# Kernel optimization log

Hardware: AMD Instinct MI355X
Metric: run time of the kernel (lower is better)

Reference implementation:

```python
import jax, jax.numpy as jnp
import numpy as np

B, S, CL, DIM, HEADS, FFN = 2, 2048, 512, 2048, 16, 8192
EPS = 1e-6


def rms_norm(x, w):
    return x * jax.lax.rsqrt(jnp.mean(x * x, axis=-1, keepdims=True) + EPS) * w


def mha(q, k, v, num_heads):
    b, sq, d = q.shape
    sk = k.shape[1]
    hd = d // num_heads
    q = q.reshape(b, sq, num_heads, hd)
    k = k.reshape(b, sk, num_heads, hd)
    v = v.reshape(b, sk, num_heads, hd)
    attn = jnp.einsum('bqhd,bkhd->bhqk', q, k) * (hd ** -0.5)
    attn = jax.nn.softmax(attn, axis=-1)
    out = jnp.einsum('bhqk,bkhd->bqhd', attn, v)
    return out.reshape(b, sq, d)


def setup_inputs() -> dict:
    key = jax.random.key(0)
    ks = iter(jax.random.split(key, 48))
    nrm = lambda shape, scale: jax.random.normal(next(ks), shape, jnp.float32) * scale
    w_scale = DIM ** -0.5
    inp = {
        'x': nrm((B, S, DIM), 1.0),
        'e': nrm((B, 6, DIM), 0.5),
        'context': nrm((B, CL, DIM), 1.0),
        'modulation': nrm((1, 6, DIM), w_scale),
        'norm1_w': jnp.ones((DIM,), jnp.float32),
        'norm2_w': jnp.ones((DIM,), jnp.float32),
        'norm3_w': jnp.ones((DIM,), jnp.float32),
        'sa_nq_w': jnp.ones((DIM,), jnp.float32),
        'sa_nk_w': jnp.ones((DIM,), jnp.float32),
        'ffn_norm_w': jnp.ones((DIM,), jnp.float32),
        'sa_qw': nrm((DIM, DIM), w_scale), 'sa_qb': jnp.zeros((DIM,), jnp.float32),
        'sa_kw': nrm((DIM, DIM), w_scale), 'sa_kb': jnp.zeros((DIM,), jnp.float32),
        'sa_vw': nrm((DIM, DIM), w_scale), 'sa_vb': jnp.zeros((DIM,), jnp.float32),
        'sa_ow': nrm((DIM, DIM), w_scale), 'sa_ob': jnp.zeros((DIM,), jnp.float32),
        'ca_qw': nrm((DIM, DIM), w_scale), 'ca_qb': jnp.zeros((DIM,), jnp.float32),
        'ca_kw': nrm((DIM, DIM), w_scale), 'ca_kb': jnp.zeros((DIM,), jnp.float32),
        'ca_vw': nrm((DIM, DIM), w_scale), 'ca_vb': jnp.zeros((DIM,), jnp.float32),
        'ca_ow': nrm((DIM, DIM), w_scale), 'ca_ob': jnp.zeros((DIM,), jnp.float32),
        'ffn_w1': nrm((DIM, FFN), w_scale), 'ffn_b1': jnp.zeros((FFN,), jnp.float32),
        'ffn_w2': nrm((FFN, DIM), FFN ** -0.5), 'ffn_b2': jnp.zeros((DIM,), jnp.float32),
    }
    return inp


def reference(x, e, context, modulation, norm1_w, norm2_w, norm3_w, sa_nq_w, sa_nk_w,
              ffn_norm_w, sa_qw, sa_qb, sa_kw, sa_kb, sa_vw, sa_vb, sa_ow, sa_ob,
              ca_qw, ca_qb, ca_kw, ca_kb, ca_vw, ca_vb, ca_ow, ca_ob,
              ffn_w1, ffn_b1, ffn_w2, ffn_b2):
    # AdaLN modulation: (modulation + e) chunked into 6 along dim=1 -> each [B,1,DIM]
    mod = modulation + e
    e0, e1, e2, e3, e4, e5 = [mod[:, i:i + 1, :] for i in range(6)]

    # --- self attention with qk_norm=True ---
    h = rms_norm(x, norm1_w) * (1.0 + e1) + e0
    q = rms_norm(h @ sa_qw + sa_qb, sa_nq_w)
    k = rms_norm(h @ sa_kw + sa_kb, sa_nk_w)
    v = h @ sa_vw + sa_vb
    y = mha(q, k, v, HEADS) @ sa_ow + sa_ob
    x = x + y * e2

    # --- cross attention (cross_attn_norm=False, no qk norm) ---
    h = rms_norm(x, norm2_w)
    q = h @ ca_qw + ca_qb
    k = context @ ca_kw + ca_kb
    v = context @ ca_vw + ca_vb
    y = mha(q, k, v, HEADS) @ ca_ow + ca_ob
    x = x + y

    # --- FFN: modulate(norm3(x)) -> RMSNorm -> Linear -> GELU(tanh) -> Linear ---
    h = rms_norm(x, norm3_w) * (1.0 + e4) + e3
    h = rms_norm(h, ffn_norm_w)
    h = jax.nn.gelu(h @ ffn_w1 + ffn_b1, approximate=True)
    y = h @ ffn_w2 + ffn_b2
    x = x + y * e5
    return x
```

## Files before the change

### kernel.cpp

```cpp
#include <hip/hip_runtime.h>
#include <hip/hip_bf16.h>
#include <cstdint>

#define DIM   2048
#define HEADS 16
#define HD    128
#define SEQ   2048
#define CLEN  512
#define FFND  8192
#define BATCH 2

using bf16 = __hip_bfloat16;
typedef __attribute__((ext_vector_type(8))) short  short8;
typedef __attribute__((ext_vector_type(4))) short  short4v;
typedef __attribute__((ext_vector_type(4))) float  f32x4;
typedef __attribute__((ext_vector_type(8))) __bf16 bf16x8;

__device__ __forceinline__ short f2bs(float f){ bf16 h = __float2bfloat16(f); return __builtin_bit_cast(short, h); }
__device__ __forceinline__ float bs2f(short s){ return __builtin_bit_cast(float, (uint32_t)((uint16_t)s) << 16); }

__device__ __forceinline__ f32x4 mfma16(short8 a, short8 b, f32x4 c){
  return __builtin_amdgcn_mfma_f32_16x16x32_bf16(
      __builtin_bit_cast(bf16x8, a), __builtin_bit_cast(bf16x8, b), c, 0, 0, 0);
}

__device__ __forceinline__ void gload_lds16(const void* g, const void* l){
  __builtin_amdgcn_global_load_lds(
      (const __attribute__((address_space(1))) void*)(uintptr_t)g,
      (__attribute__((address_space(3))) void*)(uint32_t)(uintptr_t)l, 16, 0, 0);
}

__device__ __forceinline__ float block_sum(float v, float* sbuf, int tid){
  #pragma unroll
  for (int m = 32; m >= 1; m >>= 1) v += __shfl_xor(v, m, 64);
  const int w = tid >> 6;
  if ((tid & 63) == 0) sbuf[w] = v;
  __syncthreads();
  float r = sbuf[0] + sbuf[1] + sbuf[2] + sbuf[3];
  __syncthreads();
  return r;
}


__global__ void modadd_k(const float* __restrict__ m, const float* __restrict__ e,
                         float* __restrict__ out){
  int i = blockIdx.x * 256 + threadIdx.x;
  out[i] = m[i % (6 * DIM)] + e[i];
}

__global__ void f2b8_k(const float* __restrict__ in, bf16* __restrict__ out){
  int i = blockIdx.x * 256 + threadIdx.x;
  const float4* p = (const float4*)in;
  float4 a = p[2*i], c = p[2*i+1];
  short8 o;
  o[0]=f2bs(a.x); o[1]=f2bs(a.y); o[2]=f2bs(a.z); o[3]=f2bs(a.w);
  o[4]=f2bs(c.x); o[5]=f2bs(c.y); o[6]=f2bs(c.z); o[7]=f2bs(c.w);
  *((short8*)out + i) = o;
}

__global__ void biascat_k(const float* __restrict__ b0, const float* __restrict__ b1,
                          const float* __restrict__ b2, float* __restrict__ bcat){
  int i = blockIdx.x * 256 + threadIdx.x;
  const float* src = (i < DIM) ? b0 : (i < 2*DIM) ? b1 : b2;
  bcat[i] = src[i & (DIM-1)];
}

__global__ __launch_bounds__(256) void transpose_w(const float* __restrict__ W,
                                                   bf16* __restrict__ Wt, int K, int N){
  __shared__ float tile[32][33];
  const int tx = threadIdx.x & 31, ty = threadIdx.x >> 5;
  const size_t k0 = blockIdx.y * 32, n0 = blockIdx.x * 32;
  #pragma unroll
  for (int i = 0; i < 4; i++)
    tile[ty + i*8][tx] = W[(k0 + ty + i*8) * (size_t)N + n0 + tx];
  __syncthreads();
  #pragma unroll
  for (int i = 0; i < 4; i++)
    Wt[(n0 + ty + i*8) * (size_t)K + k0 + tx] = __float2bfloat16(tile[tx][ty + i*8]);
}

template<int MODE>
__global__ __launch_bounds__(256) void norm_x(const float* __restrict__ x,
    const float* __restrict__ w1, const float* __restrict__ w2,
    const float* __restrict__ mod, bf16* __restrict__ out, int S)
{
  const int row = blockIdx.x, tid = threadIdx.x;
  const int b = row / S;
  __shared__ float sbuf[4];
  const float* xr = x + (size_t)row * DIM;
  float v[8];
  #pragma unroll
  for (int i = 0; i < 2; i++){
    float4 t = *(const float4*)(xr + i*1024 + tid*4);
    v[i*4+0]=t.x; v[i*4+1]=t.y; v[i*4+2]=t.z; v[i*4+3]=t.w;
  }
  float ss = 0.f;
  #pragma unroll
  for (int j = 0; j < 8; j++) ss += v[j]*v[j];
  ss = block_sum(ss, sbuf, tid);
  const float r = rsqrtf(ss * (1.0f/DIM) + 1e-6f);
  const float* mb = mod + (size_t)b * 6 * DIM;
  float t8[8];
  #pragma unroll
  for (int i = 0; i < 2; i++)
    #pragma unroll
    for (int j = 0; j < 4; j++){
      int n = i*1024 + tid*4 + j;
      float val = v[i*4+j] * r * w1[n];
      if (MODE == 1) val = val * (1.f + mb[DIM + n]) + mb[n];
      if (MODE == 3) val = val * (1.f + mb[4*DIM + n]) + mb[3*DIM + n];
      t8[i*4+j] = val;
    }
  if (MODE == 3){
    float s2 = 0.f;
    #pragma unroll
    for (int j = 0; j < 8; j++) s2 += t8[j]*t8[j];
    s2 = block_sum(s2, sbuf, tid);
    const float r2 = rsqrtf(s2 * (1.0f/DIM) + 1e-6f);
    #pragma unroll
    for (int i = 0; i < 2; i++)
      #pragma unroll
      for (int j = 0; j < 4; j++){
        int n = i*1024 + tid*4 + j;
        t8[i*4+j] = t8[i*4+j] * r2 * w2[n];
      }
  }
  #pragma unroll
  for (int i = 0; i < 2; i++){
    short4v o;
    #pragma unroll
    for (int j = 0; j < 4; j++) o[j] = f2bs(t8[i*4+j]);
    *(short4v*)(out + (size_t)row*DIM + i*1024 + tid*4) = o;
  }
}

__global__ __launch_bounds__(256) void rmsnorm_bf16_ip(bf16* __restrict__ x,
                                                       const float* __restrict__ w){
  const int row = blockIdx.x, tid = threadIdx.x;
  __shared__ float sbuf[4];
  bf16* xr = x + (size_t)row * DIM;
  short8 v = *(const short8*)(xr + tid*8);
  float f[8]; float ss = 0.f;
  #pragma unroll
  for (int j = 0; j < 8; j++){ f[j] = bs2f(v[j]); ss += f[j]*f[j]; }
  ss = block_sum(ss, sbuf, tid);
  const float r = rsqrtf(ss * (1.0f/DIM) + 1e-6f);
  short8 o;
  #pragma unroll
  for (int j = 0; j < 8; j++) o[j] = f2bs(f[j] * r * w[tid*8 + j]);
  *(short8*)(xr + tid*8) = o;
}

#define GBUF 24576
template<int EPI>
__global__ __launch_bounds__(512, 2) void gemm_bf16(
    const bf16* __restrict__ A, const bf16* __restrict__ Bt,
    const float* __restrict__ bias, const float* __restrict__ xin,
    const float* __restrict__ mod, float* __restrict__ outf,
    bf16* __restrict__ outb, bf16* __restrict__ out1, bf16* __restrict__ out2,
    int M, int N, int K, int S_tok, int eidx)
{
  __shared__ __align__(16) char lds[3][GBUF];
  const int tid = threadIdx.x;
  const int w = tid >> 6, l = tid & 63;
  const int lrow = l & 15, lhi = l >> 4;
  const int wm = w >> 2, wn = w & 3;
  const size_t m0 = (size_t)blockIdx.y * 128, n0 = (size_t)blockIdx.x * 256;

  f32x4 acc[4][4] = {};

  auto gofs = [&](int sid){ return (size_t)(sid >> 2) * K + (size_t)(((sid & 3) ^ ((sid >> 3) & 3)) * 8); };
  const bf16* gA0 = A  + m0 * K + gofs(tid);
  const bf16* gB0 = Bt + n0 * K + gofs(tid);
  const bf16* gB1 = Bt + n0 * K + gofs(tid + 512);

  auto stage = [&](int kt, char* buf){
    const size_t ko = (size_t)kt * 32;
    gload_lds16(gA0 + ko, buf + tid * 16);
    gload_lds16(gB0 + ko, buf + 8192 + tid * 16);
    gload_lds16(gB1 + ko, buf + 8192 + (tid + 512) * 16);
  };

  const int nt = K >> 5;
  stage(0, lds[0]);
  stage(1, lds[1]);
  asm volatile("s_waitcnt vmcnt(3)" ::: "memory");
  __builtin_amdgcn_s_barrier();
  __builtin_amdgcn_sched_barrier(0);

  const int sread = (lhi ^ ((lrow >> 1) & 3)) * 16;

  int bi = 0;
  for (int t = 0; t < nt; ++t){
    const char* br = lds[bi];
    const bool st = (t + 2 < nt);
    if (st){
      int wi = bi + 2; if (wi >= 3) wi -= 3;
      stage(t + 2, lds[wi]);
    }
    short8 af[4], bf[4];
    #pragma unroll
    for (int mi = 0; mi < 4; mi++)
      af[mi] = *(const short8*)(br + (wm*64 + mi*16 + lrow)*64 + sread);
    #pragma unroll
    for (int ni = 0; ni < 4; ni++)
      bf[ni] = *(const short8*)(br + 8192 + (wn*64 + ni*16 + lrow)*64 + sread);
    __builtin_amdgcn_s_setprio(1);
    #pragma unroll
    for (int mi = 0; mi < 4; mi++)
      #pragma unroll
      for (int ni = 0; ni < 4; ni++)
        acc[mi][ni] = mfma16(af[mi], bf[ni], acc[mi][ni]);
    __builtin_amdgcn_s_setprio(0);
    if (st)               { asm volatile("s_waitcnt vmcnt(3)" ::: "memory"); }
    else if (t + 1 < nt)  { asm volatile("s_waitcnt vmcnt(0)" ::: "memory"); }
    __builtin_amdgcn_s_barrier();
    __builtin_amdgcn_sched_barrier(0);
    bi = (bi + 1 == 3) ? 0 : bi + 1;
  }

  #pragma unroll
  for (int mi = 0; mi < 4; mi++)
    #pragma unroll
    for (int ni = 0; ni < 4; ni++)
      #pragma unroll
      for (int r = 0; r < 4; r++){
        const size_t m = m0 + wm*64 + mi*16 + lhi*4 + r;
        const size_t n = n0 + wn*64 + ni*16 + lrow;
        float v = acc[mi][ni][r] + bias[n];
        if constexpr (EPI == 0) {
          outb[m * N + n] = __float2bfloat16(v);
        } else if constexpr (EPI == 1) {
          const size_t b = m / S_tok, s = m % S_tok;
          const size_t h = n >> 7, d = n & 127;
          outb[((b*HEADS + h)*HD + d) * S_tok + s] = __float2bfloat16(v);
        } else if constexpr (EPI == 2) {
          const float ev = mod[(m / S_tok) * 6 * DIM + (size_t)eidx * DIM + n];
          outf[m * N + n] = xin[m * N + n] + v * ev;
        } else if constexpr (EPI == 3) {
          outf[m * N + n] += v;
        } else if constexpr (EPI == 4) {
          float u = 0.7978845608028654f * (v + 0.044715f * v * v * v);
          outb[m * N + n] = __float2bfloat16(0.5f * v * (1.0f + tanhf(u)));
        } else {
          const size_t sg = n >> 11, col = n & 2047;
          if (sg == 0)      outb[m * DIM + col] = __float2bfloat16(v);
          else if (sg == 1) out1[m * DIM + col] = __float2bfloat16(v);
          else {
            const size_t b = m / S_tok, s = m % S_tok;
            const size_t h = col >> 7, d = col & 127;
            out2[((b*HEADS + h)*HD + d) * S_tok + s] = __float2bfloat16(v);
          }
        }
      }
}

__global__ __launch_bounds__(256, 2) void attn_fwd(
    const bf16* __restrict__ Q, const bf16* __restrict__ Kp, const bf16* __restrict__ Vt,
    bf16* __restrict__ O, int SQ, int SKV)
{
  const int tid = threadIdx.x, w = tid >> 6, l = tid & 63;
  const int lrow = l & 15, lhi = l >> 4;
  const int nwg = gridDim.x;
  const int p = blockIdx.x;
  const int f = (p & 7) * (nwg >> 3) + (p >> 3);
  const int nqb = SQ >> 6;
  const int xq = f % nqb;
  const int h  = (f / nqb) % HEADS;
  const int b  = f / (nqb * HEADS);
  const int q0 = xq * 64 + w * 16;

  __shared__ __align__(16) char kls[2][16384];
  __shared__ __align__(16) char vls[2][16384];
  __shared__ __align__(16) bf16 P[4][16][72];
  const float scale = 0.08838834764831845f;

  const bf16* qp = Q + ((size_t)(b*SQ + q0 + lrow))*DIM + h*HD + lhi*8;
  short8 qf[4];
  #pragma unroll
  for (int ds = 0; ds < 4; ds++) qf[ds] = *(const short8*)(qp + ds*32);

  const bf16* kg = Kp + (size_t)b*SKV*DIM + h*HD;
  const bf16* vg = Vt + (size_t)(b*HEADS + h)*HD*SKV;

  f32x4 acc[8] = {};
  float m_run = -INFINITY, l_run = 0.f;
  const int nt = SKV >> 6;

  auto stage = [&](int buf, int kv0){
    char* kd = &kls[buf][0];
    #pragma unroll
    for (int i = 0; i < 4; i++){
      int sid = i*256 + tid;
      int row = sid >> 4, sg = sid & 15;
      int gsg = sg ^ (row & 7);
      gload_lds16(kg + (size_t)(kv0 + row)*DIM + gsg*8, kd + sid*16);
    }
    char* vd = &vls[buf][0];
    #pragma unroll
    for (int i = 0; i < 4; i++){
      int sid = i*256 + tid;
      int d = sid >> 3, sg = sid & 7;
      int gsg = sg ^ (d & 7);
      gload_lds16(vg + (size_t)d*SKV + kv0 + gsg*8, vd + sid*16);
    }
  };

  stage(0, 0);
  __syncthreads();

  for (int t = 0; t < nt; ++t){
    if (t + 1 < nt) stage((t + 1) & 1, (t + 1) * 64);
    const char* kb = &kls[t & 1][0];
    const char* vb = &vls[t & 1][0];

    f32x4 st[4] = {};
    #pragma unroll
    for (int kvf = 0; kvf < 4; kvf++){
      const int row = kvf*16 + lrow;
      const int rx = row & 7;
      #pragma unroll
      for (int ds = 0; ds < 4; ds++){
        const int seg = (ds*4 + lhi) ^ rx;
        short8 kf = *(const short8*)(kb + row*256 + seg*16);
        st[kvf] = mfma16(kf, qf[ds], st[kvf]);
      }
    }

    float sv[16]; float smax = -INFINITY;
    #pragma unroll
    for (int kvf = 0; kvf < 4; kvf++)
      #pragma unroll
      for (int r = 0; r < 4; r++){
        float xv = st[kvf][r] * scale;
        sv[kvf*4+r] = xv; smax = fmaxf(smax, xv);
      }
    smax = fmaxf(smax, __shfl_xor(smax, 16, 64));
    smax = fmaxf(smax, __shfl_xor(smax, 32, 64));
    const float mnew = fmaxf(m_run, smax);
    const float corr = __expf(m_run - mnew);
    float psum = 0.f;
    #pragma unroll
    for (int i = 0; i < 16; i++){ float pe = __expf(sv[i] - mnew); sv[i] = pe; psum += pe; }
    psum += __shfl_xor(psum, 16, 64); psum += __shfl_xor(psum, 32, 64);
    l_run = l_run * corr + psum;
    m_run = mnew;

    #pragma unroll
    for (int kvf = 0; kvf < 4; kvf++){
      short4v o;
      #pragma unroll
      for (int r = 0; r < 4; r++) o[r] = f2bs(sv[kvf*4+r]);
      *(short4v*)&P[w][lrow][kvf*16 + lhi*4] = o;
    }

    float cr[4];
    #pragma unroll
    for (int r = 0; r < 4; r++) cr[r] = __shfl(corr, lhi*4 + r, 64);
    #pragma unroll
    for (int df = 0; df < 8; df++){
      acc[df][0] *= cr[0]; acc[df][1] *= cr[1]; acc[df][2] *= cr[2]; acc[df][3] *= cr[3];
    }

    asm volatile("s_waitcnt lgkmcnt(0)" ::: "memory");
    __builtin_amdgcn_sched_barrier(0);

    short8 pf0 = *(const short8*)&P[w][lrow][lhi*8];
    short8 pf1 = *(const short8*)&P[w][lrow][32 + lhi*8];
    #pragma unroll
    for (int df = 0; df < 8; df++){
      const int d = df*16 + lrow;
      const int dx = d & 7;
      short8 vf0 = *(const short8*)(vb + d*128 + ((lhi)     ^ dx)*16);
      short8 vf1 = *(const short8*)(vb + d*128 + ((lhi + 4) ^ dx)*16);
      acc[df] = mfma16(pf0, vf0, acc[df]);
      acc[df] = mfma16(pf1, vf1, acc[df]);
    }
    __syncthreads();
  }

  const float linv = 1.0f / l_run;
  float li[4];
  #pragma unroll
  for (int r = 0; r < 4; r++) li[r] = __shfl(linv, lhi*4 + r, 64);
  #pragma unroll
  for (int df = 0; df < 8; df++)
    #pragma unroll
    for (int r = 0; r < 4; r++){
      const size_t q = q0 + lhi*4 + r;
      O[((size_t)(b*SQ + q))*DIM + h*HD + df*16 + lrow] = __float2bfloat16(acc[df][r] * li[r]);
    }
}


extern "C" void kernel_launch(void* const* d_in, const int* in_sizes, int n_in,
                              void* d_out, int out_size, void* d_ws, size_t ws_size,
                              hipStream_t stream)
{
  const float* x    = (const float*)d_in[0];
  const float* e    = (const float*)d_in[1];
  const float* ctx  = (const float*)d_in[2];
  const float* modw = (const float*)d_in[3];
  const float* n1w  = (const float*)d_in[4];
  const float* n2w  = (const float*)d_in[5];
  const float* n3w  = (const float*)d_in[6];
  const float* nqw  = (const float*)d_in[7];
  const float* nkw  = (const float*)d_in[8];
  const float* fnw  = (const float*)d_in[9];
  const float* saqw = (const float*)d_in[10]; const float* saqb = (const float*)d_in[11];
  const float* sakw = (const float*)d_in[12]; const float* sakb = (const float*)d_in[13];
  const float* savw = (const float*)d_in[14]; const float* savb = (const float*)d_in[15];
  const float* saow = (const float*)d_in[16]; const float* saob = (const float*)d_in[17];
  const float* caqw = (const float*)d_in[18]; const float* caqb = (const float*)d_in[19];
  const float* cakw = (const float*)d_in[20]; const float* cakb = (const float*)d_in[21];
  const float* cavw = (const float*)d_in[22]; const float* cavb = (const float*)d_in[23];
  const float* caow = (const float*)d_in[24]; const float* caob = (const float*)d_in[25];
  const float* fw1  = (const float*)d_in[26]; const float* fb1  = (const float*)d_in[27];
  const float* fw2  = (const float*)d_in[28]; const float* fb2  = (const float*)d_in[29];
  float* out = (float*)d_out;
  (void)in_sizes; (void)n_in; (void)out_size; (void)ws_size;

  char* ws = (char*)d_ws;
  size_t off = 0;
  auto alloc = [&](size_t bytes) -> void* {
    void* p = ws + off; off = (off + bytes + 255) & ~(size_t)255; return p;
  };
  bf16*  wt   = (bf16*)alloc((size_t)FFND * DIM * 2);
  float* mod  = (float*)alloc((size_t)BATCH * 6 * DIM * 4);
  float* bcat = (float*)alloc((size_t)3 * DIM * 4);
  bf16*  ctxb = (bf16*)alloc((size_t)BATCH * CLEN * DIM * 2);
  bf16*  hbuf = (bf16*)alloc((size_t)BATCH * SEQ * DIM * 2);
  bf16*  qbuf = (bf16*)alloc((size_t)BATCH * SEQ * DIM * 2);
  bf16*  kbuf = (bf16*)alloc((size_t)BATCH * SEQ * DIM * 2);
  bf16*  vtb  = (bf16*)alloc((size_t)BATCH * SEQ * DIM * 2);
  bf16*  aout = (bf16*)alloc((size_t)BATCH * SEQ * DIM * 2);
  float* xcur = (float*)alloc((size_t)BATCH * SEQ * DIM * 4);
  bf16*  hf   = (bf16*)alloc((size_t)BATCH * SEQ * FFND * 2);

  const int M = BATCH * SEQ;
  const int Mc = BATCH * CLEN;

  modadd_k<<<dim3(96), dim3(256), 0, stream>>>(modw, e, mod);
  f2b8_k<<<dim3(1024), dim3(256), 0, stream>>>(ctx, ctxb);
  biascat_k<<<dim3(24), dim3(256), 0, stream>>>(saqb, sakb, savb, bcat);

  norm_x<1><<<dim3(M), dim3(256), 0, stream>>>(x, n1w, nullptr, mod, hbuf, SEQ);

  transpose_w<<<dim3(DIM/32, DIM/32), dim3(256), 0, stream>>>(saqw, wt,                     DIM, DIM);
  transpose_w<<<dim3(DIM/32, DIM/32), dim3(256), 0, stream>>>(sakw, wt + (size_t)DIM*DIM,   DIM, DIM);
  transpose_w<<<dim3(DIM/32, DIM/32), dim3(256), 0, stream>>>(savw, wt + (size_t)2*DIM*DIM, DIM, DIM);
  gemm_bf16<5><<<dim3(3*DIM/256, M/128), dim3(512), 0, stream>>>(hbuf, wt, bcat, nullptr, nullptr, nullptr, qbuf, kbuf, vtb, M, 3*DIM, DIM, SEQ, 0);
  rmsnorm_bf16_ip<<<dim3(M), dim3(256), 0, stream>>>(qbuf, nqw);
  rmsnorm_bf16_ip<<<dim3(M), dim3(256), 0, stream>>>(kbuf, nkw);

  attn_fwd<<<dim3((SEQ/64)*HEADS*BATCH), dim3(256), 0, stream>>>(qbuf, kbuf, vtb, aout, SEQ, SEQ);

  transpose_w<<<dim3(DIM/32, DIM/32), dim3(256), 0, stream>>>(saow, wt, DIM, DIM);
  gemm_bf16<2><<<dim3(DIM/256, M/128), dim3(512), 0, stream>>>(aout, wt, saob, x, mod, xcur, nullptr, nullptr, nullptr, M, DIM, DIM, SEQ, 2);

  norm_x<2><<<dim3(M), dim3(256), 0, stream>>>(xcur, n2w, nullptr, mod, hbuf, SEQ);

  transpose_w<<<dim3(DIM/32, DIM/32), dim3(256), 0, stream>>>(caqw, wt, DIM, DIM);
  gemm_bf16<0><<<dim3(DIM/256, M/128), dim3(512), 0, stream>>>(hbuf, wt, caqb, nullptr, nullptr, nullptr, qbuf, nullptr, nullptr, M, DIM, DIM, SEQ, 0);

  transpose_w<<<dim3(DIM/32, DIM/32), dim3(256), 0, stream>>>(cakw, wt, DIM, DIM);
  gemm_bf16<0><<<dim3(DIM/256, Mc/128), dim3(512), 0, stream>>>(ctxb, wt, cakb, nullptr, nullptr, nullptr, kbuf, nullptr, nullptr, Mc, DIM, DIM, CLEN, 0);

  transpose_w<<<dim3(DIM/32, DIM/32), dim3(256), 0, stream>>>(cavw, wt, DIM, DIM);
  gemm_bf16<1><<<dim3(DIM/256, Mc/128), dim3(512), 0, stream>>>(ctxb, wt, cavb, nullptr, nullptr, nullptr, vtb, nullptr, nullptr, Mc, DIM, DIM, CLEN, 0);

  attn_fwd<<<dim3((SEQ/64)*HEADS*BATCH), dim3(256), 0, stream>>>(qbuf, kbuf, vtb, aout, SEQ, CLEN);

  transpose_w<<<dim3(DIM/32, DIM/32), dim3(256), 0, stream>>>(caow, wt, DIM, DIM);
  gemm_bf16<3><<<dim3(DIM/256, M/128), dim3(512), 0, stream>>>(aout, wt, caob, nullptr, nullptr, xcur, nullptr, nullptr, nullptr, M, DIM, DIM, SEQ, 0);

  norm_x<3><<<dim3(M), dim3(256), 0, stream>>>(xcur, n3w, fnw, mod, hbuf, SEQ);

  transpose_w<<<dim3(FFND/32, DIM/32), dim3(256), 0, stream>>>(fw1, wt, DIM, FFND);
  gemm_bf16<4><<<dim3(FFND/256, M/128), dim3(512), 0, stream>>>(hbuf, wt, fb1, nullptr, nullptr, nullptr, hf, nullptr, nullptr, M, FFND, DIM, SEQ, 0);

  transpose_w<<<dim3(DIM/32, FFND/32), dim3(256), 0, stream>>>(fw2, wt, FFND, DIM);
  gemm_bf16<2><<<dim3(DIM/256, M/128), dim3(512), 0, stream>>>(hf, wt, fb2, xcur, mod, out, nullptr, nullptr, nullptr, M, DIM, FFND, SEQ, 5);
}
```

Before: 968.1 us.

## Process 128 query rows per attention block with split K/V staging

The attention kernel now gives each wave two 16-row query groups, so each block covers 128 queries, and every K/V tile loaded into LDS is reused across twice as many queries. This halves the grid and the K/V global traffic per query. V is now single-buffered and loaded one iteration behind K, with explicit vmcnt waits and barriers in place of __syncthreads, which cuts LDS use. In exchange each thread holds twice the accumulator registers, which may lower occupancy, and there are fewer blocks to spread across the CUs.

```diff
diff --git a/kernel.cpp b/kernel.cpp
--- a/kernel.cpp
+++ b/kernel.cpp
@@ -264,30 +264,33 @@
   const int nwg = gridDim.x;
   const int p = blockIdx.x;
   const int f = (p & 7) * (nwg >> 3) + (p >> 3);
-  const int nqb = SQ >> 6;
+  const int nqb = SQ >> 7;
   const int xq = f % nqb;
   const int h  = (f / nqb) % HEADS;
   const int b  = f / (nqb * HEADS);
-  const int q0 = xq * 64 + w * 16;
+  const int q0 = xq * 128 + w * 32;
 
   __shared__ __align__(16) char kls[2][16384];
-  __shared__ __align__(16) char vls[2][16384];
-  __shared__ __align__(16) bf16 P[4][16][72];
+  __shared__ __align__(16) char vls[16384];
+  __shared__ __align__(16) bf16 P[4][2][16][72];
   const float scale = 0.08838834764831845f;
 
-  const bf16* qp = Q + ((size_t)(b*SQ + q0 + lrow))*DIM + h*HD + lhi*8;
-  short8 qf[4];
-  #pragma unroll
-  for (int ds = 0; ds < 4; ds++) qf[ds] = *(const short8*)(qp + ds*32);
+  short8 qf[2][4];
+  #pragma unroll
+  for (int g = 0; g < 2; g++){
+    const bf16* qp = Q + ((size_t)(b*SQ + q0 + g*16 + lrow))*DIM + h*HD + lhi*8;
+    #pragma unroll
+    for (int ds = 0; ds < 4; ds++) qf[g][ds] = *(const short8*)(qp + ds*32);
+  }
 
   const bf16* kg = Kp + (size_t)b*SKV*DIM + h*HD;
   const bf16* vg = Vt + (size_t)(b*HEADS + h)*HD*SKV;
 
-  f32x4 acc[8] = {};
-  float m_run = -INFINITY, l_run = 0.f;
+  f32x4 acc[2][8] = {};
+  float m_run[2] = {-INFINITY, -INFINITY}, l_run[2] = {0.f, 0.f};
   const int nt = SKV >> 6;
 
-  auto stage = [&](int buf, int kv0){
+  auto stage_k = [&](int buf, int kv0){
     char* kd = &kls[buf][0];
     #pragma unroll
     for (int i = 0; i < 4; i++){
@@ -296,25 +299,28 @@
       int gsg = sg ^ (row & 7);
       gload_lds16(kg + (size_t)(kv0 + row)*DIM + gsg*8, kd + sid*16);
     }
-    char* vd = &vls[buf][0];
+  };
+  auto stage_v = [&](int kv0){
     #pragma unroll
     for (int i = 0; i < 4; i++){
       int sid = i*256 + tid;
       int d = sid >> 3, sg = sid & 7;
       int gsg = sg ^ (d & 7);
-      gload_lds16(vg + (size_t)d*SKV + kv0 + gsg*8, vd + sid*16);
+      gload_lds16(vg + (size_t)d*SKV + kv0 + gsg*8, &vls[0] + sid*16);
     }
   };
 
-  stage(0, 0);
-  __syncthreads();
+  stage_k(0, 0);
+  stage_v(0);
+  asm volatile("s_waitcnt vmcnt(0)" ::: "memory");
+  __builtin_amdgcn_s_barrier();
 
   for (int t = 0; t < nt; ++t){
-    if (t + 1 < nt) stage((t + 1) & 1, (t + 1) * 64);
+    if (t > 0)      stage_v(t * 64);
+    if (t + 1 < nt) stage_k((t + 1) & 1, (t + 1) * 64);
     const char* kb = &kls[t & 1][0];
-    const char* vb = &vls[t & 1][0];
-
-    f32x4 st[4] = {};
+
+    f32x4 st[2][4] = {};
     #pragma unroll
     for (int kvf = 0; kvf < 4; kvf++){
       const int row = kvf*16 + lrow;
@@ -323,73 +329,89 @@
       for (int ds = 0; ds < 4; ds++){
         const int seg = (ds*4 + lhi) ^ rx;
         short8 kf = *(const short8*)(kb + row*256 + seg*16);
-        st[kvf] = mfma16(kf, qf[ds], st[kvf]);
+        st[0][kvf] = mfma16(kf, qf[0][ds], st[0][kvf]);
+        st[1][kvf] = mfma16(kf, qf[1][ds], st[1][kvf]);
       }
     }
 
-    float sv[16]; float smax = -INFINITY;
-    #pragma unroll
-    for (int kvf = 0; kvf < 4; kvf++)
-      #pragma unroll
-      for (int r = 0; r < 4; r++){
-        float xv = st[kvf][r] * scale;
-        sv[kvf*4+r] = xv; smax = fmaxf(smax, xv);
+    #pragma unroll
+    for (int g = 0; g < 2; g++){
+      float sv[16]; float smax = -INFINITY;
+      #pragma unroll
+      for (int kvf = 0; kvf < 4; kvf++)
+        #pragma unroll
+        for (int r = 0; r < 4; r++){
+          float xv = st[g][kvf][r] * scale;
+          sv[kvf*4+r] = xv; smax = fmaxf(smax, xv);
+        }
+      smax = fmaxf(smax, __shfl_xor(smax, 16, 64));
+      smax = fmaxf(smax, __shfl_xor(smax, 32, 64));
+      const float mnew = fmaxf(m_run[g], smax);
+      const float corr = __expf(m_run[g] - mnew);
+      float psum = 0.f;
+      #pragma unroll
+      for (int i = 0; i < 16; i++){ float pe = __expf(sv[i] - mnew); sv[i] = pe; psum += pe; }
+      psum += __shfl_xor(psum, 16, 64); psum += __shfl_xor(psum, 32, 64);
+      l_run[g] = l_run[g] * corr + psum;
+      m_run[g] = mnew;
+      #pragma unroll
+      for (int kvf = 0; kvf < 4; kvf++){
+        short4v o;
+        #pragma unroll
+        for (int r = 0; r < 4; r++) o[r] = f2bs(sv[kvf*4+r]);
+        *(short4v*)&P[w][g][lrow][kvf*16 + lhi*4] = o;
       }
-    smax = fmaxf(smax, __shfl_xor(smax, 16, 64));
-    smax = fmaxf(smax, __shfl_xor(smax, 32, 64));
-    const float mnew = fmaxf(m_run, smax);
-    const float corr = __expf(m_run - mnew);
-    float psum = 0.f;
-    #pragma unroll
-    for (int i = 0; i < 16; i++){ float pe = __expf(sv[i] - mnew); sv[i] = pe; psum += pe; }
-    psum += __shfl_xor(psum, 16, 64); psum += __shfl_xor(psum, 32, 64);
-    l_run = l_run * corr + psum;
-    m_run = mnew;
-
-    #pragma unroll
-    for (int kvf = 0; kvf < 4; kvf++){
-      short4v o;
-      #pragma unroll
-      for (int r = 0; r < 4; r++) o[r] = f2bs(sv[kvf*4+r]);
-      *(short4v*)&P[w][lrow][kvf*16 + lhi*4] = o;
-    }
-
-    float cr[4];
-    #pragma unroll
-    for (int r = 0; r < 4; r++) cr[r] = __shfl(corr, lhi*4 + r, 64);
-    #pragma unroll
-    for (int df = 0; df < 8; df++){
-      acc[df][0] *= cr[0]; acc[df][1] *= cr[1]; acc[df][2] *= cr[2]; acc[df][3] *= cr[3];
-    }
-
+      float cr[4];
+      #pragma unroll
+      for (int r = 0; r < 4; r++) cr[r] = __shfl(corr, lhi*4 + r, 64);
+      #pragma unroll
+      for (int df = 0; df < 8; df++){
+        acc[g][df][0] *= cr[0]; acc[g][df][1] *= cr[1];
+        acc[g][df][2] *= cr[2]; acc[g][df][3] *= cr[3];
+      }
+    }
+
+    if (t + 1 < nt) { asm volatile("s_waitcnt vmcnt(4)" ::: "memory"); }
+    else            { asm volatile("s_waitcnt vmcnt(0)" ::: "memory"); }
+    __builtin_amdgcn_s_barrier();
     asm volatile("s_waitcnt lgkmcnt(0)" ::: "memory");
     __builtin_amdgcn_sched_barrier(0);
 
-    short8 pf0 = *(const short8*)&P[w][lrow][lhi*8];
-    short8 pf1 = *(const short8*)&P[w][lrow][32 + lhi*8];
+    short8 pf[2][2];
+    #pragma unroll
+    for (int g = 0; g < 2; g++){
+      pf[g][0] = *(const short8*)&P[w][g][lrow][lhi*8];
+      pf[g][1] = *(const short8*)&P[w][g][lrow][32 + lhi*8];
+    }
     #pragma unroll
     for (int df = 0; df < 8; df++){
       const int d = df*16 + lrow;
       const int dx = d & 7;
-      short8 vf0 = *(const short8*)(vb + d*128 + ((lhi)     ^ dx)*16);
-      short8 vf1 = *(const short8*)(vb + d*128 + ((lhi + 4) ^ dx)*16);
-      acc[df] = mfma16(pf0, vf0, acc[df]);
-      acc[df] = mfma16(pf1, vf1, acc[df]);
-    }
-    __syncthreads();
-  }
-
-  const float linv = 1.0f / l_run;
-  float li[4];
-  #pragma unroll
-  for (int r = 0; r < 4; r++) li[r] = __shfl(linv, lhi*4 + r, 64);
-  #pragma unroll
-  for (int df = 0; df < 8; df++)
-    #pragma unroll
-    for (int r = 0; r < 4; r++){
-      const size_t q = q0 + lhi*4 + r;
-      O[((size_t)(b*SQ + q))*DIM + h*HD + df*16 + lrow] = __float2bfloat16(acc[df][r] * li[r]);
-    }
+      short8 vf0 = *(const short8*)(&vls[0] + d*128 + ((lhi)     ^ dx)*16);
+      short8 vf1 = *(const short8*)(&vls[0] + d*128 + ((lhi + 4) ^ dx)*16);
+      acc[0][df] = mfma16(pf[0][0], vf0, acc[0][df]);
+      acc[0][df] = mfma16(pf[0][1], vf1, acc[0][df]);
+      acc[1][df] = mfma16(pf[1][0], vf0, acc[1][df]);
+      acc[1][df] = mfma16(pf[1][1], vf1, acc[1][df]);
+    }
+    if (t + 1 < nt) { asm volatile("s_waitcnt vmcnt(0)" ::: "memory"); }
+    __builtin_amdgcn_s_barrier();
+  }
+
+  #pragma unroll
+  for (int g = 0; g < 2; g++){
+    const float linv = 1.0f / l_run[g];
+    float li[4];
+    #pragma unroll
+    for (int r = 0; r < 4; r++) li[r] = __shfl(linv, lhi*4 + r, 64);
+    #pragma unroll
+    for (int df = 0; df < 8; df++)
+      #pragma unroll
+      for (int r = 0; r < 4; r++){
+        const size_t q = q0 + g*16 + lhi*4 + r;
+        O[((size_t)(b*SQ + q))*DIM + h*HD + df*16 + lrow] = __float2bfloat16(acc[g][df][r] * li[r]);
+      }
+  }
 }
 
 
@@ -453,7 +475,7 @@
   rmsnorm_bf16_ip<<<dim3(M), dim3(256), 0, stream>>>(qbuf, nqw);
   rmsnorm_bf16_ip<<<dim3(M), dim3(256), 0, stream>>>(kbuf, nkw);
 
-  attn_fwd<<<dim3((SEQ/64)*HEADS*BATCH), dim3(256), 0, stream>>>(qbuf, kbuf, vtb, aout, SEQ, SEQ);
+  attn_fwd<<<dim3((SEQ/128)*HEADS*BATCH), dim3(256), 0, stream>>>(qbuf, kbuf, vtb, aout, SEQ, SEQ);
 
   transpose_w<<<dim3(DIM/32, DIM/32), dim3(256), 0, stream>>>(saow, wt, DIM, DIM);
   gemm_bf16<2><<<dim3(DIM/256, M/128), dim3(512), 0, stream>>>(aout, wt, saob, x, mod, xcur, nullptr, nullptr, nullptr, M, DIM, DIM, SEQ, 2);
@@ -469,7 +491,7 @@
   transpose_w<<<dim3(DIM/32, DIM/32), dim3(256), 0, stream>>>(cavw, wt, DIM, DIM);
   gemm_bf16<1><<<dim3(DIM/256, Mc/128), dim3(512), 0, stream>>>(ctxb, wt, cavb, nullptr, nullptr, nullptr, vtb, nullptr, nullptr, Mc, DIM, DIM, CLEN, 0);
 
-  attn_fwd<<<dim3((SEQ/64)*HEADS*BATCH), dim3(256), 0, stream>>>(qbuf, kbuf, vtb, aout, SEQ, CLEN);
+  attn_fwd<<<dim3((SEQ/128)*HEADS*BATCH), dim3(256), 0, stream>>>(qbuf, kbuf, vtb, aout, SEQ, CLEN);
 
   transpose_w<<<dim3(DIM/32, DIM/32), dim3(256), 0, stream>>>(caow, wt, DIM, DIM);
   gemm_bf16<3><<<dim3(DIM/256, M/128), dim3(512), 0, stream>>>(aout, wt, caob, nullptr, nullptr, xcur, nullptr, nullptr, nullptr, M, DIM, DIM, SEQ, 0);
```

New measurement: 939.5 us. -3.0%, faster.
